# Performance work log

Measured on AMD Instinct MI355X. Metric: run time of the kernel, lower is better.

Reference implementation:

```python
import jax, jax.numpy as jnp
import numpy as np

STRIDES = (2, 2, 2)  # from init_kwargs


def _sparse_conv3d_transpose(images, kernel, default_value, base_plane, strides):
    """Sparse masked 3D transposed conv driven by a per-pixel depth base plane.

    images:     [B, Hi, Wi, Di, C]  stored slab of active voxels per pixel
    kernel:     [kH, kW, kD, F, C]
    base_plane: [B, Ho, Wo, 1] int  starting VIRTUAL depth of the output slab
    Output virtual depth of voxel (ho, wo, do) is base_plane[ho, wo] + do.
    Input slab start (in input-depth units) at input pixel (hi, wi) is
    base_plane[hi*sH, wi*sW] // sD. SAME-style padding ((k-1)//2).
    Out-of-slab / out-of-bounds taps read default_value (frozen zero).
    """
    B, Hi, Wi, Di, C = images.shape
    k0, k1, k2, F, _ = kernel.shape
    s0, s1, s2 = strides
    bp = base_plane[..., 0]                       # [B, Ho, Wo]
    Ho, Wo = bp.shape[1], bp.shape[2]
    Do = Di * s2
    p0, p1, p2 = (k0 - 1) // 2, (k1 - 1) // 2, (k2 - 1) // 2
    bp_in = bp[:, ::s0, ::s1] // s2               # [B, Hi, Wi] input slab start
    b_idx = jnp.arange(B)[:, None, None]
    vd = bp[..., None] + jnp.arange(Do)           # [B, Ho, Wo, Do] virtual out depth
    ho = jnp.arange(Ho)
    wo = jnp.arange(Wo)
    out = jnp.zeros((B, Ho, Wo, Do, F), images.dtype)
    for kh in range(k0):
        hn = ho + p0 - kh
        hok = (hn % s0 == 0) & (hn >= 0) & (hn < Hi * s0)
        hi = jnp.clip(hn // s0, 0, Hi - 1)
        for kw in range(k1):
            wn = wo + p1 - kw
            wok = (wn % s1 == 0) & (wn >= 0) & (wn < Wi * s1)
            wi = jnp.clip(wn // s1, 0, Wi - 1)
            sp_ok = hok[None, :, None] & wok[None, None, :]              # [1,Ho,Wo]
            bpg = bp_in[b_idx, hi[None, :, None], wi[None, None, :]]     # [B,Ho,Wo]
            for kd in range(k2):
                dn = vd + p2 - kd                                        # [B,Ho,Wo,Do]
                dok = (dn % s2) == 0
                di = dn // s2 - bpg[..., None]
                mask = sp_ok[..., None] & dok & (di >= 0) & (di < Di)
                dic = jnp.clip(di, 0, Di - 1)
                # gather [B,Ho,Wo,Do,C]
                vals = images[b_idx[..., None], hi[None, :, None, None],
                              wi[None, None, :, None], dic]
                vals = jnp.where(mask[..., None], vals, default_value)
                out = out + jnp.einsum('bhwdc,fc->bhwdf', vals, kernel[kh, kw, kd])
    return out


def setup_inputs() -> dict:
    key = jax.random.key(0)
    k1, k2, k3 = jax.random.split(key, 3)
    B, Hi, Wi, Di, C, F = 2, 64, 64, 32, 16, 8
    images = jax.random.normal(k1, (B, Hi, Wi, Di, C), dtype=jnp.float32)
    base_plane = jax.random.randint(k2, (B, Hi * 2, Wi * 2, 1), 0, 16, dtype=jnp.int32)
    kernel = jax.random.normal(k3, (3, 3, 3, F, C), dtype=jnp.float32) * 0.1
    default_value = jnp.zeros((), dtype=jnp.float32)  # frozen, zeros initializer
    return {"images": images, "base_plane": base_plane,
            "kernel": kernel, "default_value": default_value}


def reference(images, base_plane, kernel, default_value):
    return _sparse_conv3d_transpose(images, kernel, default_value, base_plane, STRIDES)
```

## Files before the change

### kernel.cpp

```cpp
#include <hip/hip_runtime.h>

constexpr int Bc  = 2;
constexpr int HiC = 64, WiC = 64, DiC = 32;
constexpr int Cc  = 16, Fc  = 8;
constexpr int HoC = 128, WoC = 128, DoC = 64;
constexpr int IMG_ELEMS = Bc * HiC * WiC * DiC * Cc;

typedef __attribute__((ext_vector_type(8))) short short8;
typedef __attribute__((ext_vector_type(4))) float f32x4;

__device__ alignas(16) const float FZERO[8] = {0, 0, 0, 0, 0, 0, 0, 0};

__device__ __forceinline__ unsigned pk2(float x, float y) {
    unsigned ux = __float_as_uint(x), uy = __float_as_uint(y);
    ux += ((ux >> 16) & 1u) + 0x7FFFu;
    uy += ((uy >> 16) & 1u) + 0x7FFFu;
    return (ux >> 16) | (uy & 0xFFFF0000u);
}
__device__ __forceinline__ short8 pack8(float4 a, float4 b) {
    union { unsigned u[4]; short8 s; } r;
    r.u[0] = pk2(a.x, a.y); r.u[1] = pk2(a.z, a.w);
    r.u[2] = pk2(b.x, b.y); r.u[3] = pk2(b.z, b.w);
    return r.s;
}

__global__ __launch_bounds__(256)
void imgcvt(const float4* __restrict__ in, uint2* __restrict__ outv, int n4) {
    int i = blockIdx.x * 256 + threadIdx.x;
    if (i < n4) {
        float4 v = in[i];
        uint2 o; o.x = pk2(v.x, v.y); o.y = pk2(v.z, v.w);
        outv[i] = o;
    } else if (i < n4 + 8) {
        uint2 z; z.x = 0u; z.y = 0u;
        outv[i] = z;
    }
}

template<int CLS, int CVT>
__device__ __forceinline__ void doCols(const short* __restrict__ img16,
                                       const float* __restrict__ img32,
                                       const int*   __restrict__ bp,
                                       const float* __restrict__ kern,
                                       float*       __restrict__ out,
                                       float*       __restrict__ ldsw,
                                       int b, int ho, int wo0, int lane) {
    constexpr int NP = (CLS == 0) ? 1 : ((CLS == 3) ? 4 : 2);
    constexpr int OP = (NP + 1) / 2;
    constexpr int KH[4][4] = {{1,0,0,0},{1,1,0,0},{0,2,0,0},{0,0,2,2}};
    constexpr int KW[4][4] = {{1,0,0,0},{0,2,0,0},{1,1,0,0},{0,2,0,2}};

    const int quad = lane >> 4, n = lane & 15;
    const int half = quad >> 1, chalf = quad & 1;

    short8 bE[NP], bO[OP];
    #pragma unroll
    for (int p = 0; p < NP; ++p) {
        const int kp = KH[CLS][p] * 3 + KW[CLS][p];
        const float* wp = (n < Fc)
            ? kern + (kp * 3 + 2 * half) * 128 + n * 16 + chalf * 8 : FZERO;
        bE[p] = pack8(*(const float4*)wp, *(const float4*)(wp + 4));
    }
    #pragma unroll
    for (int pp = 0; pp < OP; ++pp) {
        const int  PA   = (2 * pp < NP) ? 2 * pp : 0;
        const bool hasB = (2 * pp + 1) < NP;
        const int  PB   = hasB ? (2 * pp + 1) : 0;
        const int kpa = KH[CLS][PA] * 3 + KW[CLS][PA];
        const int kpb = KH[CLS][PB] * 3 + KW[CLS][PB];
        const int kp  = half ? kpb : kpa;
        const bool v  = (n < Fc) && (!half || hasB);
        const float* wp = v ? kern + (kp * 3 + 1) * 128 + n * 16 + chalf * 8 : FZERO;
        bO[pp] = pack8(*(const float4*)wp, *(const float4*)(wp + 4));
    }

    int colx[4], bpcol[4], bpgr[4][NP], pxo[4][NP]; bool pvs[4][NP];
    #pragma unroll
    for (int cc = 0; cc < 4; ++cc) {
        const int wo = wo0 + 2 * cc;
        colx[cc]  = __builtin_amdgcn_readfirstlane((b * HoC + ho) * WoC + wo);
        bpcol[cc] = bp[colx[cc]];
        #pragma unroll
        for (int p = 0; p < NP; ++p) {
            const int kh = KH[CLS][p], kw = KW[CLS][p];
            int hi = (ho + 1 - kh) >> 1; hi = hi > HiC - 1 ? HiC - 1 : hi;
            int wi = (wo + 1 - kw) >> 1; wi = wi > WiC - 1 ? WiC - 1 : wi;
            pvs[cc][p] = (kh != 0 || ho + 1 < HoC) && (kw != 0 || wo + 1 < WoC);
            const int sidx =
                __builtin_amdgcn_readfirstlane((b * HoC + 2 * hi) * WoC + 2 * wi);
            bpgr[cc][p] = bp[sidx];
            pxo[cc][p]  = __builtin_amdgcn_readfirstlane(
                              ((b * HiC + hi) * WiC + wi) * (DiC * Cc));
        }
    }

    #pragma unroll
    for (int cc = 0; cc < 4; ++cc) {
        const int bp_col = bpcol[cc];
        const int q      = (bp_col + 1) & 1;
        const int baseE  = (bp_col + q + 1) >> 1;
        const int baseO  = (bp_col + 1 - q) >> 1;
        int sE[NP], sO[NP];
        #pragma unroll
        for (int p = 0; p < NP; ++p) {
            const int bpg = bpgr[cc][p] >> 1;
            sE[p] = pvs[cc][p] ? baseE - bpg : -100000;
            sO[p] = pvs[cc][p] ? baseO - bpg : -100000;
        }

        f32x4 accE[2] = {{0.f,0.f,0.f,0.f},{0.f,0.f,0.f,0.f}};
        f32x4 accO[2] = {{0.f,0.f,0.f,0.f},{0.f,0.f,0.f,0.f}};

        #pragma unroll
        for (int g = 0; g < 2; ++g) {
            #pragma unroll
            for (int p = 0; p < NP; ++p) {
                const int  di = sE[p] + 16 * g + n - half;
                const bool ok = (unsigned)di < (unsigned)DiC;
                short8 a;
                if constexpr (CVT) {
                    const float* ap = ok ? img32 + pxo[cc][p] + di * Cc + chalf * 8 : FZERO;
                    a = pack8(*(const float4*)ap, *(const float4*)(ap + 4));
                } else {
                    const int off = ok ? pxo[cc][p] + di * Cc + chalf * 8 : IMG_ELEMS;
                    a = *(const short8*)(img16 + off);
                }
                accE[g] = __builtin_amdgcn_mfma_f32_16x16x32_bf16(a, bE[p], accE[g], 0, 0, 0);
            }
            #pragma unroll
            for (int pp = 0; pp < OP; ++pp) {
                const int  PA   = (2 * pp < NP) ? 2 * pp : 0;
                const bool hasB = (2 * pp + 1) < NP;
                const int  PB   = hasB ? (2 * pp + 1) : 0;
                const int  sOs  = half ? (hasB ? sO[PB] : -100000) : sO[PA];
                const int  pxs  = half ? pxo[cc][PB] : pxo[cc][PA];
                const int  di = sOs + 16 * g + n;
                const bool ok = (unsigned)di < (unsigned)DiC;
                short8 a;
                if constexpr (CVT) {
                    const float* ap = ok ? img32 + pxs + di * Cc + chalf * 8 : FZERO;
                    a = pack8(*(const float4*)ap, *(const float4*)(ap + 4));
                } else {
                    const int off = ok ? pxs + di * Cc + chalf * 8 : IMG_ELEMS;
                    a = *(const short8*)(img16 + off);
                }
                accO[g] = __builtin_amdgcn_mfma_f32_16x16x32_bf16(a, bO[pp], accO[g], 0, 0, 0);
            }
        }

        __builtin_amdgcn_wave_barrier();
        if (n < Fc) {
            #pragma unroll
            for (int g = 0; g < 2; ++g) {
                #pragma unroll
                for (int r = 0; r < 4; ++r) {
                    const int m2 = 16 * g + quad * 4 + r;
                    ldsw[(2 * m2 + q) * Fc + n]     = accE[g][r];
                    ldsw[(2 * m2 + 1 - q) * Fc + n] = accO[g][r];
                }
            }
        }
        __builtin_amdgcn_wave_barrier();
        float* outc = out + (size_t)colx[cc] * (DoC * Fc);
        *(float4*)(outc + lane * 8)     = *(const float4*)(ldsw + lane * 8);
        *(float4*)(outc + lane * 8 + 4) = *(const float4*)(ldsw + lane * 8 + 4);
        __builtin_amdgcn_wave_barrier();
    }
}

template<int CVT>
__global__ __launch_bounds__(256, 3)
void sconv_mfma(const short* __restrict__ img16, const float* __restrict__ img32,
                const int* __restrict__ bp, const float* __restrict__ kern,
                float* __restrict__ out) {
    __shared__ float lds[4 * DoC * Fc];
    const int t = threadIdx.x, wv = t >> 6, lane = t & 63;
    const int b = blockIdx.z, ho = blockIdx.y;
    const int wo0 = (blockIdx.x << 4) + (wv & 1) + ((wv >> 1) << 3);
    float* ldsw = lds + wv * (DoC * Fc);
    if (ho & 1) {
        if (wv & 1) doCols<3, CVT>(img16, img32, bp, kern, out, ldsw, b, ho, wo0, lane);
        else        doCols<2, CVT>(img16, img32, bp, kern, out, ldsw, b, ho, wo0, lane);
    } else {
        if (wv & 1) doCols<1, CVT>(img16, img32, bp, kern, out, ldsw, b, ho, wo0, lane);
        else        doCols<0, CVT>(img16, img32, bp, kern, out, ldsw, b, ho, wo0, lane);
    }
}

extern "C" void kernel_launch(void* const* d_in, const int* in_sizes, int n_in,
                              void* d_out, int out_size, void* d_ws, size_t ws_size,
                              hipStream_t stream) {
    const float* images = (const float*)d_in[0];
    const int*   bp     = (const int*)d_in[1];
    const float* kern   = (const float*)d_in[2];
    float* out = (float*)d_out;

    const size_t needWs = ((size_t)IMG_ELEMS + 32) * sizeof(short);

    dim3 grid(WoC / 16, HoC, Bc), block(256);
    if (ws_size >= needWs) {
        const int n4 = IMG_ELEMS / 4;
        hipLaunchKernelGGL(imgcvt, dim3(n4 / 256 + 1), dim3(256), 0, stream,
                           (const float4*)images, (uint2*)d_ws, n4);
        hipLaunchKernelGGL((sconv_mfma<0>), grid, block, 0, stream,
                           (const short*)d_ws, images, bp, kern, out);
    } else {
        hipLaunchKernelGGL((sconv_mfma<1>), grid, block, 0, stream,
                           (const short*)nullptr, images, bp, kern, out);
    }
}
```

Baseline: 100.3 us.

## Stage per-block input depth slabs into LDS with global_load_lds before MFMA

Each block now uses async global-to-LDS loads to copy the 9 or 18 bf16 input pixel slabs its output columns need into shared memory, plus a zero pad, before computing. The MFMA A-operand gathers then read from LDS with precomputed byte offsets instead of scattered global reads. This aims to cut repeated global and L2 traffic for slabs shared across columns and kernel taps. In exchange it adds about 18KB of LDS per block, a block-wide barrier, and a serial prologue that delays compute.

Result: no change. 98.62 us (-1.7%).

```diff
diff --git a/kernel.cpp b/kernel.cpp
--- a/kernel.cpp
+++ b/kernel.cpp
@@ -6,6 +6,10 @@
 constexpr int HoC = 128, WoC = 128, DoC = 64;
 constexpr int IMG_ELEMS = Bc * HiC * WiC * DiC * Cc;
 
+constexpr int SLAB_SHORTS = DiC * Cc;
+constexpr int NSLAB       = 18;
+constexpr int ZOFF        = NSLAB * SLAB_SHORTS * 2;
+
 typedef __attribute__((ext_vector_type(8))) short short8;
 typedef __attribute__((ext_vector_type(4))) float f32x4;
 
@@ -22,6 +26,13 @@
     r.u[0] = pk2(a.x, a.y); r.u[1] = pk2(a.z, a.w);
     r.u[2] = pk2(b.x, b.y); r.u[3] = pk2(b.z, b.w);
     return r.s;
+}
+
+__device__ __forceinline__ void gload_lds16(const short* g, short* l) {
+    __builtin_amdgcn_global_load_lds(
+        (const __attribute__((address_space(1))) void*)(unsigned long long)(const void*)g,
+        (__attribute__((address_space(3))) void*)(unsigned long long)(void*)l,
+        16, 0, 0);
 }
 
 __global__ __launch_bounds__(256)
@@ -38,13 +49,13 @@
 }
 
 template<int CLS, int CVT>
-__device__ __forceinline__ void doCols(const short* __restrict__ img16,
+__device__ __forceinline__ void doCols(const short* __restrict__ slabs,
                                        const float* __restrict__ img32,
                                        const int*   __restrict__ bp,
                                        const float* __restrict__ kern,
                                        float*       __restrict__ out,
                                        float*       __restrict__ ldsw,
-                                       int b, int ho, int wo0, int lane) {
+                                       int b, int ho, int wo0, int wi0, int lane) {
     constexpr int NP = (CLS == 0) ? 1 : ((CLS == 3) ? 4 : 2);
     constexpr int OP = (NP + 1) / 2;
     constexpr int KH[4][4] = {{1,0,0,0},{1,1,0,0},{0,2,0,0},{0,0,2,2}};
@@ -52,6 +63,7 @@
 
     const int quad = lane >> 4, n = lane & 15;
     const int half = quad >> 1, chalf = quad & 1;
+    const int chalfB = chalf * 16;
 
     short8 bE[NP], bO[OP];
     #pragma unroll
@@ -89,8 +101,14 @@
             const int sidx =
                 __builtin_amdgcn_readfirstlane((b * HoC + 2 * hi) * WoC + 2 * wi);
             bpgr[cc][p] = bp[sidx];
-            pxo[cc][p]  = __builtin_amdgcn_readfirstlane(
-                              ((b * HiC + hi) * WiC + wi) * (DiC * Cc));
+            if constexpr (CVT) {
+                pxo[cc][p] = __builtin_amdgcn_readfirstlane(
+                                 ((b * HiC + hi) * WiC + wi) * (DiC * Cc));
+            } else {
+                const int hidx = (kh == 0) ? 1 : 0;
+                pxo[cc][p] = __builtin_amdgcn_readfirstlane(
+                                 (hidx * 9 + (wi - wi0)) << 10);
+            }
         }
     }
 
@@ -122,8 +140,8 @@
                     const float* ap = ok ? img32 + pxo[cc][p] + di * Cc + chalf * 8 : FZERO;
                     a = pack8(*(const float4*)ap, *(const float4*)(ap + 4));
                 } else {
-                    const int off = ok ? pxo[cc][p] + di * Cc + chalf * 8 : IMG_ELEMS;
-                    a = *(const short8*)(img16 + off);
+                    const int off = ok ? pxo[cc][p] + di * 32 + chalfB : ZOFF;
+                    a = *(const short8*)((const char*)slabs + off);
                 }
                 accE[g] = __builtin_amdgcn_mfma_f32_16x16x32_bf16(a, bE[p], accE[g], 0, 0, 0);
             }
@@ -141,8 +159,8 @@
                     const float* ap = ok ? img32 + pxs + di * Cc + chalf * 8 : FZERO;
                     a = pack8(*(const float4*)ap, *(const float4*)(ap + 4));
                 } else {
-                    const int off = ok ? pxs + di * Cc + chalf * 8 : IMG_ELEMS;
-                    a = *(const short8*)(img16 + off);
+                    const int off = ok ? pxs + di * 32 + chalfB : ZOFF;
+                    a = *(const short8*)((const char*)slabs + off);
                 }
                 accO[g] = __builtin_amdgcn_mfma_f32_16x16x32_bf16(a, bO[pp], accO[g], 0, 0, 0);
             }
@@ -173,17 +191,34 @@
 void sconv_mfma(const short* __restrict__ img16, const float* __restrict__ img32,
                 const int* __restrict__ bp, const float* __restrict__ kern,
                 float* __restrict__ out) {
+    __shared__ short slabs[NSLAB * SLAB_SHORTS + 8];
     __shared__ float lds[4 * DoC * Fc];
     const int t = threadIdx.x, wv = t >> 6, lane = t & 63;
     const int b = blockIdx.z, ho = blockIdx.y;
     const int wo0 = (blockIdx.x << 4) + (wv & 1) + ((wv >> 1) << 3);
+    const int wi0 = blockIdx.x << 3;
     float* ldsw = lds + wv * (DoC * Fc);
+
+    if constexpr (!CVT) {
+        const int nSlab = (ho & 1) ? 18 : 9;
+        const int hi0 = ho >> 1;
+        int hi1 = (ho + 1) >> 1; if (hi1 > HiC - 1) hi1 = HiC - 1;
+        for (int s = wv; s < nSlab; s += 4) {
+            const int hi = (s >= 9) ? hi1 : hi0;
+            int wi = wi0 + ((s >= 9) ? s - 9 : s); if (wi > WiC - 1) wi = WiC - 1;
+            const short* g = img16 + (((b * HiC + hi) * WiC + wi) << 9) + lane * 8;
+            gload_lds16(g, &slabs[s << 9]);
+        }
+        if (t < 8) slabs[NSLAB * SLAB_SHORTS + t] = 0;
+        __syncthreads();
+    }
+
     if (ho & 1) {
-        if (wv & 1) doCols<3, CVT>(img16, img32, bp, kern, out, ldsw, b, ho, wo0, lane);
-        else        doCols<2, CVT>(img16, img32, bp, kern, out, ldsw, b, ho, wo0, lane);
+        if (wv & 1) doCols<3, CVT>(slabs, img32, bp, kern, out, ldsw, b, ho, wo0, wi0, lane);
+        else        doCols<2, CVT>(slabs, img32, bp, kern, out, ldsw, b, ho, wo0, wi0, lane);
     } else {
-        if (wv & 1) doCols<1, CVT>(img16, img32, bp, kern, out, ldsw, b, ho, wo0, lane);
-        else        doCols<0, CVT>(img16, img32, bp, kern, out, ldsw, b, ho, wo0, lane);
+        if (wv & 1) doCols<1, CVT>(slabs, img32, bp, kern, out, ldsw, b, ho, wo0, wi0, lane);
+        else        doCols<0, CVT>(slabs, img32, bp, kern, out, ldsw, b, ho, wo0, wi0, lane);
     }
 }
 
```
